# Performance work log

Measured on AMD Instinct MI355X. Metric: run time of the kernel, lower is better.

Reference implementation:

```python
import jax, jax.numpy as jnp
import numpy as np

NUM_HEADS = 8
NEG_INF = float(-2**32 + 1)
LN_EPS = 1e-8


def setup_inputs() -> dict:
    key = jax.random.key(0)
    ks = jax.random.split(key, 9)
    B, T, D = 4, 2048, 512
    inp = {
        "queries": jax.random.normal(ks[0], (B, T, D), jnp.float32),
        "keys": jax.random.normal(ks[1], (B, T, D), jnp.float32),
        "values": jax.random.normal(ks[2], (B, T, D), jnp.float32),
        "Wq": jax.random.normal(ks[3], (D, D), jnp.float32) / np.sqrt(D),
        "bq": jnp.zeros((D,), jnp.float32),
        "Wk": jax.random.normal(ks[4], (D, D), jnp.float32) / np.sqrt(D),
        "bk": jnp.zeros((D,), jnp.float32),
        "Wv": jax.random.normal(ks[5], (D, D), jnp.float32) / np.sqrt(D),
        "bv": jnp.zeros((D,), jnp.float32),
        "gamma": jnp.ones((D,), jnp.float32),
        "beta": jnp.zeros((D,), jnp.float32),
    }
    return inp


def _split_heads(x, h):
    # torch.cat(torch.chunk(x, h, dim=2), dim=0): [B,T,D] -> [h*B, T, D/h], head-major
    B, T, D = x.shape
    return x.reshape(B, T, h, D // h).transpose(2, 0, 1, 3).reshape(h * B, T, D // h)


def _merge_heads(x, h, B):
    # inverse: [h*B, T, dh] -> [B, T, h*dh]
    hB, T, dh = x.shape
    return x.reshape(h, B, T, dh).transpose(1, 2, 0, 3).reshape(B, T, h * dh)


def reference(queries, keys, values, Wq, bq, Wk, bk, Wv, bv, gamma, beta):
    h = NUM_HEADS
    B, Tq, D = queries.shape
    dh = D // h

    Q = jax.nn.relu(queries @ Wq + bq)
    K = jax.nn.relu(keys @ Wk + bk)
    V = jax.nn.relu(values @ Wv + bv)

    Q_ = _split_heads(Q, h)  # [h*B, Tq, dh]
    K_ = _split_heads(K, h)
    V_ = _split_heads(V, h)

    scores = jnp.einsum('bqd,bkd->bqk', Q_, K_) / jnp.sqrt(jnp.float32(dh))  # [h*B, Tq, Tk]

    # key padding mask: zero rows in `keys` get -inf scores
    key_mask = jnp.sign(jnp.abs(jnp.sum(keys, axis=-1)))  # [B, Tk]
    key_mask = jnp.tile(key_mask, (h, 1))  # [h*B, Tk]
    scores = jnp.where(key_mask[:, None, :] == 0.0, NEG_INF, scores)

    attn = jax.nn.softmax(scores, axis=-1)

    # query mask applied multiplicatively post-softmax
    query_mask = jnp.sign(jnp.abs(jnp.sum(queries, axis=-1)))  # [B, Tq]
    query_mask = jnp.tile(query_mask, (h, 1))  # [h*B, Tq]
    attn = attn * query_mask[:, :, None]

    out = jnp.einsum('bqk,bkd->bqd', attn, V_)  # [h*B, Tq, dh]
    out = _merge_heads(out, h, B) + queries  # residual

    # custom LayerNorm: torch.std is unbiased (ddof=1), eps added to std
    mean = out.mean(-1, keepdims=True)
    std = jnp.sqrt(out.var(-1, ddof=1, keepdims=True))
    return gamma * (out - mean) / (std + LN_EPS) + beta
```

## Files before the change

kernel.cpp:

```cpp
#include <hip/hip_runtime.h>


typedef __attribute__((ext_vector_type(8))) __bf16 bf16x8;
typedef __attribute__((ext_vector_type(4))) float f32x4;

#if __has_builtin(__builtin_amdgcn_exp2f)
#define EXP2F __builtin_amdgcn_exp2f
#else
#define EXP2F exp2f
#endif

#define QSCALE (0.125f * 1.4426950408889634f)

__device__ __forceinline__ unsigned short f2bf(float f) {
  return __builtin_bit_cast(unsigned short, (__bf16)f);
}
__device__ __forceinline__ unsigned pk2(float a, float b) {
  return (unsigned)f2bf(a) | ((unsigned)f2bf(b) << 16);
}
__device__ __forceinline__ f32x4 mfma16(bf16x8 a, bf16x8 b, f32x4 c) {
  return __builtin_amdgcn_mfma_f32_16x16x32_bf16(a, b, c, 0, 0, 0);
}
__device__ __forceinline__ bf16x8 ld_bf8(const unsigned short* p) {
  return *(const bf16x8*)p;
}
__device__ __forceinline__ void g2l16(const void* g, void* l) {
  __builtin_amdgcn_global_load_lds(
      (const __attribute__((address_space(1))) void*)g,
      (__attribute__((address_space(3))) void*)l, 16, 0, 0);
}

__global__ __launch_bounds__(256) void wt_kernel(const float* __restrict__ Wq,
                                                 const float* __restrict__ Wk,
                                                 const float* __restrict__ Wv,
                                                 unsigned short* __restrict__ Wt) {
  int idx = blockIdx.x * 256 + threadIdx.x;
  int o = idx * 8;
  int z = o >> 18;
  int rem = o & 262143;
  int n = rem >> 9;
  int k0 = rem & 511;
  const float* W = (z == 0) ? Wq : ((z == 1) ? Wk : Wv);
  unsigned int w[4];
#pragma unroll
  for (int i = 0; i < 4; ++i) {
    unsigned short lo = f2bf(W[(k0 + 2 * i) * 512 + n]);
    unsigned short hi = f2bf(W[(k0 + 2 * i + 1) * 512 + n]);
    w[i] = (unsigned)lo | ((unsigned)hi << 16);
  }
  *(uint4*)(Wt + o) = make_uint4(w[0], w[1], w[2], w[3]);
}

__global__ __launch_bounds__(256, 3) void proj_kernel(
    const float* __restrict__ Xq, const float* __restrict__ Xk,
    const float* __restrict__ Xv, const float* __restrict__ bq,
    const float* __restrict__ bk, const float* __restrict__ bv,
    const unsigned short* __restrict__ Wt, unsigned short* __restrict__ Qb,
    unsigned short* __restrict__ Kb, unsigned short* __restrict__ Vt,
    float* __restrict__ qmask, float* __restrict__ kmask) {
  __shared__ float Asm[2][128][16];
  __shared__ unsigned short Bsm[128][32];

  int tid = threadIdx.x;
  int m0g = blockIdx.x * 128;
  int z = m0g >> 13;
  int m0 = m0g & 8191;
  int n0 = blockIdx.y * 128;
  const float* X = (z == 0) ? Xq : ((z == 1) ? Xk : Xv);
  const float* bias = (z == 0) ? bq : ((z == 1) ? bk : bv);
  const unsigned short* Wz = Wt + z * 262144;

  int w = tid >> 6, lane = tid & 63;
  int wm = w >> 1, wn = w & 1;
  int mrow = lane & 15, quad = lane >> 4;

  int srow = tid >> 2, schk = tid & 3;
  const float* gA = X + (m0 + srow) * 512 + schk * 4;
  const unsigned short* gB = Wz + (n0 + srow) * 512 + schk * 8;
  char* lA = (char*)&Asm[0][0][0] + tid * 16;
  char* lB = (char*)&Bsm[0][0] + tid * 16;

  const float* rA = &Asm[quad >> 1][0][(quad & 1) * 8];
  const unsigned short* rB = &Bsm[0][quad * 8];

  f32x4 zero = {0.f, 0.f, 0.f, 0.f};
  f32x4 acc[4][4];
#pragma unroll
  for (int i = 0; i < 4; ++i)
#pragma unroll
    for (int j = 0; j < 4; ++j) acc[i][j] = zero;

  bool domask = (z < 2) && (n0 == 0) && (wn == 0);
  float rsum[4] = {0.f, 0.f, 0.f, 0.f};

  for (int kc = 0; kc < 16; ++kc) {
    int ko = kc * 32;
    g2l16(gA + ko, lA);
    g2l16(gA + ko + 64 * 512, lA + 4096);
    g2l16(gA + ko + 16, lA + 8192);
    g2l16(gA + ko + 16 + 64 * 512, lA + 12288);
    g2l16(gB + ko, lB);
    g2l16(gB + ko + 64 * 512, lB + 4096);
    __syncthreads();

    bf16x8 af[4], bfr[4];
#pragma unroll
    for (int mt = 0; mt < 4; ++mt) {
      const float* pa = rA + (wm * 64 + mt * 16 + mrow) * 16;
      f32x4 lo = *(const f32x4*)pa;
      f32x4 hi = *(const f32x4*)(pa + 4);
      if (domask)
        rsum[mt] += lo[0] + lo[1] + lo[2] + lo[3] + hi[0] + hi[1] + hi[2] + hi[3];
      bf16x8 t;
      t[0] = (__bf16)lo[0]; t[1] = (__bf16)lo[1];
      t[2] = (__bf16)lo[2]; t[3] = (__bf16)lo[3];
      t[4] = (__bf16)hi[0]; t[5] = (__bf16)hi[1];
      t[6] = (__bf16)hi[2]; t[7] = (__bf16)hi[3];
      af[mt] = t;
    }
#pragma unroll
    for (int nt = 0; nt < 4; ++nt)
      bfr[nt] = ld_bf8(rB + (wn * 64 + nt * 16 + mrow) * 32);
#pragma unroll
    for (int mt = 0; mt < 4; ++mt)
#pragma unroll
      for (int nt = 0; nt < 4; ++nt)
        acc[mt][nt] = mfma16(af[mt], bfr[nt], acc[mt][nt]);
    __syncthreads();
  }

  if (domask) {
    float* msk = (z == 0) ? qmask : kmask;
#pragma unroll
    for (int mt = 0; mt < 4; ++mt) {
      float s = rsum[mt];
      s += __shfl_xor(s, 16);
      s += __shfl_xor(s, 32);
      if (quad == 0)
        msk[m0 + wm * 64 + mt * 16 + mrow] = (s == 0.f) ? 0.f : 1.f;
    }
  }

  if (z < 2) {
    unsigned short* dst = (z == 0) ? Qb : Kb;
    float sc = (z == 0) ? QSCALE : 1.0f;
#pragma unroll
    for (int nt = 0; nt < 4; ++nt) {
      int n = n0 + wn * 64 + nt * 16 + mrow;
      float bv_ = bias[n];
#pragma unroll
      for (int mt = 0; mt < 4; ++mt) {
        int m = m0 + wm * 64 + mt * 16 + quad * 4;
#pragma unroll
        for (int r = 0; r < 4; ++r) {
          float v = fmaxf(acc[mt][nt][r] + bv_, 0.f) * sc;
          dst[(m + r) * 512 + n] = f2bf(v);
        }
      }
    }
  } else {
#pragma unroll
    for (int nt = 0; nt < 4; ++nt) {
      int n = n0 + wn * 64 + nt * 16 + mrow;
      int hh = n >> 6, jj = n & 63;
      float bv_ = bias[n];
#pragma unroll
      for (int mt = 0; mt < 4; ++mt) {
        int grow = m0 + wm * 64 + mt * 16 + quad * 4;
        int bb = grow >> 11, tl = grow & 2047;
        int pos = (tl & ~31) + quad * 8 + (mt & 1) * 4;
        float p0 = fmaxf(acc[mt][nt][0] + bv_, 0.f);
        float p1 = fmaxf(acc[mt][nt][1] + bv_, 0.f);
        float p2 = fmaxf(acc[mt][nt][2] + bv_, 0.f);
        float p3 = fmaxf(acc[mt][nt][3] + bv_, 0.f);
        *(uint2*)(Vt + ((hh * 4 + bb) * 64 + jj) * 2048 + pos) =
            make_uint2(pk2(p0, p1), pk2(p2, p3));
      }
    }
  }
}

__global__ __launch_bounds__(256, 2) void attn_kernel(
    const unsigned short* __restrict__ Qb, const unsigned short* __restrict__ Kb,
    const unsigned short* __restrict__ Vt, const float* __restrict__ qmask,
    const float* __restrict__ kmask, const float* __restrict__ queries,
    float* __restrict__ out) {
  __shared__ char smem[66560];
  unsigned short* KsmS = (unsigned short*)smem;
  unsigned short* VsmS = (unsigned short*)(smem + 32768);
  float* Obuf = (float*)smem;
  float* lbuf = (float*)(smem + 65536);

  int hb = blockIdx.x;
  int qt = blockIdx.y;
  int h = hb >> 2, b = hb & 3;
  int q0 = qt * 128;
  int tid = threadIdx.x;
  int w = tid >> 6, lane = tid & 63;
  int qh = w >> 1, kh2 = w & 1;
  int mrow = lane & 15, quad = lane >> 4;

  const unsigned short* gK =
      Kb + (b * 2048 + (tid >> 3)) * 512 + h * 64 + (((tid & 7) ^ ((tid >> 3) & 7)) * 8);
  const unsigned short* gV =
      Vt + (hb * 64 + (tid >> 4)) * 2048 + (((tid & 15) ^ ((tid >> 4) & 15)) * 8);

  bf16x8 qf[4][2];
  {
    const unsigned short* qp =
        Qb + (b * 2048 + q0 + qh * 64 + mrow) * 512 + h * 64 + quad * 8;
#pragma unroll
    for (int qn = 0; qn < 4; ++qn) {
      qf[qn][0] = ld_bf8(qp + qn * 8192);
      qf[qn][1] = ld_bf8(qp + qn * 8192 + 32);
    }
  }

  f32x4 zero = {0.f, 0.f, 0.f, 0.f};
  f32x4 oacc[4][4];
#pragma unroll
  for (int i = 0; i < 4; ++i)
#pragma unroll
    for (int j = 0; j < 4; ++j) oacc[i][j] = zero;
  float lpart[4] = {0.f, 0.f, 0.f, 0.f};

  const float* kmB = kmask + b * 2048 + kh2 * 64 + quad * 4;
  const int kfrow = kh2 * 64;
  const int mlow = mrow & 7;

#pragma unroll
  for (int j = 0; j < 4; ++j) {
    g2l16(gK + j * 32 * 512, &KsmS[j * 2048 + tid * 8]);
    g2l16(gV + j * 16 * 2048, &VsmS[j * 2048 + tid * 8]);
  }

  for (int it = 0; it < 16; ++it) {
    int bi = it & 1;
    int kb = it * 128;
    __syncthreads();

    if (it < 15) {
      int nkb = kb + 128;
      int nb = 1 - bi;
#pragma unroll
      for (int j = 0; j < 4; ++j) {
        g2l16(gK + (nkb + j * 32) * 512, &KsmS[nb * 8192 + j * 2048 + tid * 8]);
        g2l16(gV + nkb + j * 16 * 2048, &VsmS[nb * 8192 + j * 2048 + tid * 8]);
      }
    }

    f32x4 kmv[4];
#pragma unroll
    for (int mt = 0; mt < 4; ++mt)
      kmv[mt] = *(const f32x4*)(kmB + kb + mt * 16);

#pragma unroll
    for (int kg = 0; kg < 2; ++kg) {
      bf16x8 kfA0 = ld_bf8(&KsmS[bi * 8192 + (kfrow + kg * 32 + mrow) * 64 +
                                 ((quad) ^ mlow) * 8]);
      bf16x8 kfA1 = ld_bf8(&KsmS[bi * 8192 + (kfrow + kg * 32 + mrow) * 64 +
                                 ((4 + quad) ^ mlow) * 8]);
      bf16x8 kfB0 = ld_bf8(&KsmS[bi * 8192 + (kfrow + kg * 32 + 16 + mrow) * 64 +
                                 ((quad) ^ mlow) * 8]);
      bf16x8 kfB1 = ld_bf8(&KsmS[bi * 8192 + (kfrow + kg * 32 + 16 + mrow) * 64 +
                                 ((4 + quad) ^ mlow) * 8]);
      bf16x8 vfg[4];
#pragma unroll
      for (int dt = 0; dt < 4; ++dt)
        vfg[dt] = ld_bf8(&VsmS[bi * 8192 + (dt * 16 + mrow) * 128 +
                               ((kh2 * 8 + kg * 4 + quad) ^ mrow) * 8]);

      f32x4 sA[4], sB[4];
#pragma unroll
      for (int qn = 0; qn < 4; ++qn) {
        f32x4 s0 = mfma16(kfA0, qf[qn][0], zero);
        sA[qn] = mfma16(kfA1, qf[qn][1], s0);
        f32x4 s1 = mfma16(kfB0, qf[qn][0], zero);
        sB[qn] = mfma16(kfB1, qf[qn][1], s1);
      }
#pragma unroll
      for (int qn = 0; qn < 4; ++qn) {
        f32x4 p0, p1;
#pragma unroll
        for (int r = 0; r < 4; ++r) {
          p0[r] = EXP2F(sA[qn][r]) * kmv[kg * 2][r];
          p1[r] = EXP2F(sB[qn][r]) * kmv[kg * 2 + 1][r];
        }
        lpart[qn] += p0[0] + p0[1] + p0[2] + p0[3] + p1[0] + p1[1] + p1[2] + p1[3];
        bf16x8 pf = __builtin_bit_cast(
            bf16x8, make_uint4(pk2(p0[0], p0[1]), pk2(p0[2], p0[3]),
                               pk2(p1[0], p1[1]), pk2(p1[2], p1[3])));
#pragma unroll
        for (int dt = 0; dt < 4; ++dt)
          oacc[dt][qn] = mfma16(pf, vfg[dt], oacc[dt][qn]);
      }
    }
  }

#pragma unroll
  for (int qn = 0; qn < 4; ++qn) {
    lpart[qn] += __shfl_xor(lpart[qn], 16);
    lpart[qn] += __shfl_xor(lpart[qn], 32);
  }
  __syncthreads();
  if (quad == 0) {
#pragma unroll
    for (int qn = 0; qn < 4; ++qn)
      lbuf[kh2 * 128 + qh * 64 + qn * 16 + mrow] = lpart[qn];
  }
  if (kh2 == 1) {
#pragma unroll
    for (int dt = 0; dt < 4; ++dt)
#pragma unroll
      for (int qn = 0; qn < 4; ++qn)
#pragma unroll
        for (int r = 0; r < 4; ++r)
          Obuf[(qh * 64 + qn * 16 + quad * 4 + r) * 65 + dt * 16 + mrow] =
              oacc[dt][qn][r];
  }
  __syncthreads();
  if (kh2 == 0) {
#pragma unroll
    for (int qn = 0; qn < 4; ++qn) {
#pragma unroll
      for (int r = 0; r < 4; ++r) {
        int qrow = qh * 64 + qn * 16 + quad * 4 + r;
        float l = lbuf[qrow] + lbuf[128 + qrow];
        int qg = b * 2048 + q0 + qrow;
        float inv = qmask[qg] / l;
#pragma unroll
        for (int dt = 0; dt < 4; ++dt) {
          int idx = qg * 512 + h * 64 + dt * 16 + mrow;
          out[idx] =
              (oacc[dt][qn][r] + Obuf[qrow * 65 + dt * 16 + mrow]) * inv +
              queries[idx];
        }
      }
    }
  }
}

__global__ __launch_bounds__(256) void ln_kernel(float* __restrict__ out,
                                                 const float* __restrict__ gamma,
                                                 const float* __restrict__ beta) {
  int row = blockIdx.x * 4 + (threadIdx.x >> 6);
  int lane = threadIdx.x & 63;
  float* p = out + row * 512;
  float4 v1 = ((const float4*)p)[lane];
  float4 v2 = ((const float4*)p)[64 + lane];
  float s = v1.x + v1.y + v1.z + v1.w + v2.x + v2.y + v2.z + v2.w;
  float sq = v1.x * v1.x + v1.y * v1.y + v1.z * v1.z + v1.w * v1.w +
             v2.x * v2.x + v2.y * v2.y + v2.z * v2.z + v2.w * v2.w;
#pragma unroll
  for (int off = 32; off > 0; off >>= 1) {
    s += __shfl_xor(s, off);
    sq += __shfl_xor(sq, off);
  }
  float mean = s * (1.f / 512.f);
  float var = fmaxf((sq - 512.f * mean * mean) * (1.f / 511.f), 0.f);
  float inv = 1.f / (sqrtf(var) + 1e-8f);
  float4 g1 = ((const float4*)gamma)[lane];
  float4 g2 = ((const float4*)gamma)[64 + lane];
  float4 b1 = ((const float4*)beta)[lane];
  float4 b2 = ((const float4*)beta)[64 + lane];
  v1.x = g1.x * (v1.x - mean) * inv + b1.x;
  v1.y = g1.y * (v1.y - mean) * inv + b1.y;
  v1.z = g1.z * (v1.z - mean) * inv + b1.z;
  v1.w = g1.w * (v1.w - mean) * inv + b1.w;
  v2.x = g2.x * (v2.x - mean) * inv + b2.x;
  v2.y = g2.y * (v2.y - mean) * inv + b2.y;
  v2.z = g2.z * (v2.z - mean) * inv + b2.z;
  v2.w = g2.w * (v2.w - mean) * inv + b2.w;
  ((float4*)p)[lane] = v1;
  ((float4*)p)[64 + lane] = v2;
}

extern "C" void kernel_launch(void* const* d_in, const int* in_sizes, int n_in,
                              void* d_out, int out_size, void* d_ws, size_t ws_size,
                              hipStream_t stream) {
  (void)in_sizes; (void)n_in; (void)out_size; (void)ws_size;
  const float* queries = (const float*)d_in[0];
  const float* keys    = (const float*)d_in[1];
  const float* values  = (const float*)d_in[2];
  const float* Wq = (const float*)d_in[3];
  const float* bq = (const float*)d_in[4];
  const float* Wk = (const float*)d_in[5];
  const float* bk = (const float*)d_in[6];
  const float* Wv = (const float*)d_in[7];
  const float* bv = (const float*)d_in[8];
  const float* gamma = (const float*)d_in[9];
  const float* beta  = (const float*)d_in[10];
  float* out = (float*)d_out;

  char* ws = (char*)d_ws;
  unsigned short* Qb = (unsigned short*)(ws);
  unsigned short* Kb = (unsigned short*)(ws + 8 * 1024 * 1024);
  unsigned short* Vt = (unsigned short*)(ws + 16 * 1024 * 1024);
  unsigned short* Wt = (unsigned short*)(ws + 24 * 1024 * 1024);
  float* qmask = (float*)(ws + 24 * 1024 * 1024 + 3 * 512 * 512 * 2);
  float* kmask = qmask + 8192;

  wt_kernel<<<384, 256, 0, stream>>>(Wq, Wk, Wv, Wt);
  proj_kernel<<<dim3(192, 4), 256, 0, stream>>>(queries, keys, values, bq, bk, bv,
                                                Wt, Qb, Kb, Vt, qmask, kmask);
  attn_kernel<<<dim3(32, 16), 256, 0, stream>>>(Qb, Kb, Vt, qmask, kmask, queries, out);
  ln_kernel<<<2048, 256, 0, stream>>>(out, gamma, beta);
}
```

Before: 190.7 us.

## Double attention block threads, fold key mask into MFMA bias, MFMA row sums

The attention kernel now runs 512 threads per block, with each wave owning 32 query rows instead of 64, so each wave holds fewer accumulators and occupancy can rise. The key mask becomes an additive bias (-1e30 for padded keys) that seeds the score MFMA accumulator, replacing the per-element multiply after exp. Softmax denominators are accumulated with an MFMA against a ones vector instead of scalar adds and shuffles. The projection kernel's A tile in LDS is re-laid out with an XOR swizzle to cut bank conflicts. Risks: the row sum now uses bf16-rounded probabilities, and the new thread/wave index mapping must still cover the same tiles.

Measured after the change: 193.4 us. No clear change (+1.4%).

```diff
diff --git a/kernel.cpp b/kernel.cpp
--- a/kernel.cpp
+++ b/kernel.cpp
@@ -57,8 +57,8 @@
     const float* __restrict__ bk, const float* __restrict__ bv,
     const unsigned short* __restrict__ Wt, unsigned short* __restrict__ Qb,
     unsigned short* __restrict__ Kb, unsigned short* __restrict__ Vt,
-    float* __restrict__ qmask, float* __restrict__ kmask) {
-  __shared__ float Asm[2][128][16];
+    float* __restrict__ qmask, float* __restrict__ kbias) {
+  __shared__ float Asm[128][32];
   __shared__ unsigned short Bsm[128][32];
 
   int tid = threadIdx.x;
@@ -73,14 +73,16 @@
   int w = tid >> 6, lane = tid & 63;
   int wm = w >> 1, wn = w & 1;
   int mrow = lane & 15, quad = lane >> 4;
+  int m7 = mrow & 7;
+
+  int arow = tid >> 3, aslot = tid & 7;
+  const float* gA = X + (m0 + arow) * 512 + ((aslot ^ (arow & 7)) * 4);
+  char* lA = (char*)&Asm[0][0] + tid * 16;
 
   int srow = tid >> 2, schk = tid & 3;
-  const float* gA = X + (m0 + srow) * 512 + schk * 4;
   const unsigned short* gB = Wz + (n0 + srow) * 512 + schk * 8;
-  char* lA = (char*)&Asm[0][0][0] + tid * 16;
   char* lB = (char*)&Bsm[0][0] + tid * 16;
 
-  const float* rA = &Asm[quad >> 1][0][(quad & 1) * 8];
   const unsigned short* rB = &Bsm[0][quad * 8];
 
   f32x4 zero = {0.f, 0.f, 0.f, 0.f};
@@ -95,10 +97,8 @@
 
   for (int kc = 0; kc < 16; ++kc) {
     int ko = kc * 32;
-    g2l16(gA + ko, lA);
-    g2l16(gA + ko + 64 * 512, lA + 4096);
-    g2l16(gA + ko + 16, lA + 8192);
-    g2l16(gA + ko + 16 + 64 * 512, lA + 12288);
+#pragma unroll
+    for (int j = 0; j < 4; ++j) g2l16(gA + ko + j * 32 * 512, lA + j * 4096);
     g2l16(gB + ko, lB);
     g2l16(gB + ko + 64 * 512, lB + 4096);
     __syncthreads();
@@ -106,9 +106,9 @@
     bf16x8 af[4], bfr[4];
 #pragma unroll
     for (int mt = 0; mt < 4; ++mt) {
-      const float* pa = rA + (wm * 64 + mt * 16 + mrow) * 16;
-      f32x4 lo = *(const f32x4*)pa;
-      f32x4 hi = *(const f32x4*)(pa + 4);
+      const float* pa = &Asm[wm * 64 + mt * 16 + mrow][0];
+      f32x4 lo = *(const f32x4*)(pa + ((2 * quad) ^ m7) * 4);
+      f32x4 hi = *(const f32x4*)(pa + ((2 * quad + 1) ^ m7) * 4);
       if (domask)
         rsum[mt] += lo[0] + lo[1] + lo[2] + lo[3] + hi[0] + hi[1] + hi[2] + hi[3];
       bf16x8 t;
@@ -130,14 +130,20 @@
   }
 
   if (domask) {
-    float* msk = (z == 0) ? qmask : kmask;
+    float* msk = (z == 0) ? qmask : kbias;
 #pragma unroll
     for (int mt = 0; mt < 4; ++mt) {
       float s = rsum[mt];
       s += __shfl_xor(s, 16);
       s += __shfl_xor(s, 32);
-      if (quad == 0)
-        msk[m0 + wm * 64 + mt * 16 + mrow] = (s == 0.f) ? 0.f : 1.f;
+      if (quad == 0) {
+        float v;
+        if (z == 0)
+          v = (s == 0.f) ? 0.f : 1.f;
+        else
+          v = (s == 0.f) ? -1.0e30f : 0.f;
+        msk[m0 + wm * 64 + mt * 16 + mrow] = v;
+      }
     }
   }
 
@@ -180,10 +186,10 @@
   }
 }
 
-__global__ __launch_bounds__(256, 2) void attn_kernel(
+__global__ __launch_bounds__(512, 4) void attn_kernel(
     const unsigned short* __restrict__ Qb, const unsigned short* __restrict__ Kb,
     const unsigned short* __restrict__ Vt, const float* __restrict__ qmask,
-    const float* __restrict__ kmask, const float* __restrict__ queries,
+    const float* __restrict__ kbias, const float* __restrict__ queries,
     float* __restrict__ out) {
   __shared__ char smem[66560];
   unsigned short* KsmS = (unsigned short*)smem;
@@ -205,33 +211,37 @@
   const unsigned short* gV =
       Vt + (hb * 64 + (tid >> 4)) * 2048 + (((tid & 15) ^ ((tid >> 4) & 15)) * 8);
 
-  bf16x8 qf[4][2];
+  bf16x8 qf[2][2];
   {
     const unsigned short* qp =
-        Qb + (b * 2048 + q0 + qh * 64 + mrow) * 512 + h * 64 + quad * 8;
-#pragma unroll
-    for (int qn = 0; qn < 4; ++qn) {
+        Qb + (b * 2048 + q0 + qh * 32 + mrow) * 512 + h * 64 + quad * 8;
+#pragma unroll
+    for (int qn = 0; qn < 2; ++qn) {
       qf[qn][0] = ld_bf8(qp + qn * 8192);
       qf[qn][1] = ld_bf8(qp + qn * 8192 + 32);
     }
   }
 
+  bf16x8 onev;
+#pragma unroll
+  for (int i = 0; i < 8; ++i) onev[i] = (__bf16)1.0f;
+
   f32x4 zero = {0.f, 0.f, 0.f, 0.f};
-  f32x4 oacc[4][4];
+  f32x4 oacc[4][2];
 #pragma unroll
   for (int i = 0; i < 4; ++i)
 #pragma unroll
-    for (int j = 0; j < 4; ++j) oacc[i][j] = zero;
-  float lpart[4] = {0.f, 0.f, 0.f, 0.f};
-
-  const float* kmB = kmask + b * 2048 + kh2 * 64 + quad * 4;
+    for (int j = 0; j < 2; ++j) oacc[i][j] = zero;
+  f32x4 lacc[2] = {zero, zero};
+
+  const float* kmB = kbias + b * 2048 + kh2 * 64 + quad * 4;
   const int kfrow = kh2 * 64;
   const int mlow = mrow & 7;
 
 #pragma unroll
-  for (int j = 0; j < 4; ++j) {
-    g2l16(gK + j * 32 * 512, &KsmS[j * 2048 + tid * 8]);
-    g2l16(gV + j * 16 * 2048, &VsmS[j * 2048 + tid * 8]);
+  for (int j = 0; j < 2; ++j) {
+    g2l16(gK + j * 64 * 512, &KsmS[j * 4096 + tid * 8]);
+    g2l16(gV + j * 32 * 2048, &VsmS[j * 4096 + tid * 8]);
   }
 
   for (int it = 0; it < 16; ++it) {
@@ -243,9 +253,9 @@
       int nkb = kb + 128;
       int nb = 1 - bi;
 #pragma unroll
-      for (int j = 0; j < 4; ++j) {
-        g2l16(gK + (nkb + j * 32) * 512, &KsmS[nb * 8192 + j * 2048 + tid * 8]);
-        g2l16(gV + nkb + j * 16 * 2048, &VsmS[nb * 8192 + j * 2048 + tid * 8]);
+      for (int j = 0; j < 2; ++j) {
+        g2l16(gK + (nkb + j * 64) * 512, &KsmS[nb * 8192 + j * 4096 + tid * 8]);
+        g2l16(gV + nkb + j * 32 * 2048, &VsmS[nb * 8192 + j * 4096 + tid * 8]);
       }
     }
 
@@ -270,26 +280,26 @@
         vfg[dt] = ld_bf8(&VsmS[bi * 8192 + (dt * 16 + mrow) * 128 +
                                ((kh2 * 8 + kg * 4 + quad) ^ mrow) * 8]);
 
-      f32x4 sA[4], sB[4];
-#pragma unroll
-      for (int qn = 0; qn < 4; ++qn) {
-        f32x4 s0 = mfma16(kfA0, qf[qn][0], zero);
+      f32x4 sA[2], sB[2];
+#pragma unroll
+      for (int qn = 0; qn < 2; ++qn) {
+        f32x4 s0 = mfma16(kfA0, qf[qn][0], kmv[kg * 2]);
         sA[qn] = mfma16(kfA1, qf[qn][1], s0);
-        f32x4 s1 = mfma16(kfB0, qf[qn][0], zero);
+        f32x4 s1 = mfma16(kfB0, qf[qn][0], kmv[kg * 2 + 1]);
         sB[qn] = mfma16(kfB1, qf[qn][1], s1);
       }
 #pragma unroll
-      for (int qn = 0; qn < 4; ++qn) {
+      for (int qn = 0; qn < 2; ++qn) {
         f32x4 p0, p1;
 #pragma unroll
         for (int r = 0; r < 4; ++r) {
-          p0[r] = EXP2F(sA[qn][r]) * kmv[kg * 2][r];
-          p1[r] = EXP2F(sB[qn][r]) * kmv[kg * 2 + 1][r];
+          p0[r] = EXP2F(sA[qn][r]);
+          p1[r] = EXP2F(sB[qn][r]);
         }
-        lpart[qn] += p0[0] + p0[1] + p0[2] + p0[3] + p1[0] + p1[1] + p1[2] + p1[3];
         bf16x8 pf = __builtin_bit_cast(
             bf16x8, make_uint4(pk2(p0[0], p0[1]), pk2(p0[2], p0[3]),
                                pk2(p1[0], p1[1]), pk2(p1[2], p1[3])));
+        lacc[qn] = mfma16(pf, onev, lacc[qn]);
 #pragma unroll
         for (int dt = 0; dt < 4; ++dt)
           oacc[dt][qn] = mfma16(pf, vfg[dt], oacc[dt][qn]);
@@ -297,34 +307,31 @@
     }
   }
 
-#pragma unroll
-  for (int qn = 0; qn < 4; ++qn) {
-    lpart[qn] += __shfl_xor(lpart[qn], 16);
-    lpart[qn] += __shfl_xor(lpart[qn], 32);
-  }
   __syncthreads();
-  if (quad == 0) {
-#pragma unroll
-    for (int qn = 0; qn < 4; ++qn)
-      lbuf[kh2 * 128 + qh * 64 + qn * 16 + mrow] = lpart[qn];
+  if (mrow == 0) {
+#pragma unroll
+    for (int qn = 0; qn < 2; ++qn)
+#pragma unroll
+      for (int r = 0; r < 4; ++r)
+        lbuf[kh2 * 128 + qh * 32 + qn * 16 + quad * 4 + r] = lacc[qn][r];
   }
   if (kh2 == 1) {
 #pragma unroll
     for (int dt = 0; dt < 4; ++dt)
 #pragma unroll
-      for (int qn = 0; qn < 4; ++qn)
+      for (int qn = 0; qn < 2; ++qn)
 #pragma unroll
         for (int r = 0; r < 4; ++r)
-          Obuf[(qh * 64 + qn * 16 + quad * 4 + r) * 65 + dt * 16 + mrow] =
+          Obuf[(qh * 32 + qn * 16 + quad * 4 + r) * 65 + dt * 16 + mrow] =
               oacc[dt][qn][r];
   }
   __syncthreads();
   if (kh2 == 0) {
 #pragma unroll
-    for (int qn = 0; qn < 4; ++qn) {
+    for (int qn = 0; qn < 2; ++qn) {
 #pragma unroll
       for (int r = 0; r < 4; ++r) {
-        int qrow = qh * 64 + qn * 16 + quad * 4 + r;
+        int qrow = qh * 32 + qn * 16 + quad * 4 + r;
         float l = lbuf[qrow] + lbuf[128 + qrow];
         int qg = b * 2048 + q0 + qrow;
         float inv = qmask[qg] / l;
@@ -398,11 +405,11 @@
   unsigned short* Vt = (unsigned short*)(ws + 16 * 1024 * 1024);
   unsigned short* Wt = (unsigned short*)(ws + 24 * 1024 * 1024);
   float* qmask = (float*)(ws + 24 * 1024 * 1024 + 3 * 512 * 512 * 2);
-  float* kmask = qmask + 8192;
+  float* kbias = qmask + 8192;
 
   wt_kernel<<<384, 256, 0, stream>>>(Wq, Wk, Wv, Wt);
   proj_kernel<<<dim3(192, 4), 256, 0, stream>>>(queries, keys, values, bq, bk, bv,
-                                                Wt, Qb, Kb, Vt, qmask, kmask);
-  attn_kernel<<<dim3(32, 16), 256, 0, stream>>>(Qb, Kb, Vt, qmask, kmask, queries, out);
+                                                Wt, Qb, Kb, Vt, qmask, kbias);
+  attn_kernel<<<dim3(32, 16), 512, 0, stream>>>(Qb, Kb, Vt, qmask, kbias, queries, out);
   ln_kernel<<<2048, 256, 0, stream>>>(out, gamma, beta);
 }
```
